# Optimization experiments

Measured on AMD Instinct MI355X. Metric: run time of the kernel, lower is better.

Reference implementation:

```python
import jax, jax.numpy as jnp
import numpy as np

NS, B, T, S, H, V, G = 30, 16, 8, 400, 400, 20000, 3


def setup_inputs() -> dict:
    key = jax.random.key(0)
    ks = jax.random.split(key, 16)
    f = lambda k, shp, s: jax.random.normal(k, shp, jnp.float32) * s
    return dict(
        encoded_hidden=f(ks[0], (B, H), 1.0),
        encoded_outputs=f(ks[1], (B, S, H), 1.0),
        slot_emb=f(ks[2], (NS, H), 0.1),
        emb=f(ks[3], (V, H), 0.1),
        W_ih=f(ks[4], (3 * H, H), 0.05),
        W_hh=f(ks[5], (3 * H, H), 0.05),
        b_ih=jnp.zeros((3 * H,), jnp.float32),
        b_hh=jnp.zeros((3 * H,), jnp.float32),
        W_ratio_w=f(ks[6], (1, 3 * H), 0.05),
        W_ratio_b=jnp.zeros((1,), jnp.float32),
        W_gate_w=f(ks[7], (G, H), 0.05),
        W_gate_b=jnp.zeros((G,), jnp.float32),
        story=jax.random.randint(ks[8], (B, S), 0, V),
        target=jax.random.randint(ks[9], (B, NS, T), 0, V),
        encoded_lens=jax.random.randint(ks[10], (B,), S // 2, S + 1).astype(jnp.int32),
    )


def reference(encoded_hidden, encoded_outputs, slot_emb, emb, W_ih, W_hh, b_ih, b_hh,
              W_ratio_w, W_ratio_b, W_gate_w, W_gate_b, story, target, encoded_lens):
    ns, h = slot_emb.shape
    b, s, _ = encoded_outputs.shape
    t = target.shape[2]
    v = emb.shape[0]
    bs = ns * b  # fused slot*batch decode rows (parallel_decode)

    enc_out = jnp.tile(encoded_outputs, (ns, 1, 1))            # [bs,S,H]
    story_r = jnp.tile(story, (ns, 1))                          # [bs,S]
    lens_r = jnp.tile(encoded_lens, (ns,))                      # [bs]
    mask = jnp.arange(s)[None, :] < lens_r[:, None]             # [bs,S]
    h0 = jnp.tile(encoded_hidden, (ns, 1))                      # [bs,H]
    x0 = jnp.broadcast_to(slot_emb[:, None, :], (ns, b, h)).reshape(bs, h)
    # teacher-forcing inputs, slot-major flatten like target[:, :, wi].T.flatten()
    tf_in = emb[jnp.transpose(target, (2, 1, 0)).reshape(t, bs)]  # [T,bs,H]
    row = jnp.arange(bs)[:, None]
    neg_inf = jnp.float32(-jnp.inf)

    def gru_cell(x, hid):
        gi = x @ W_ih.T + b_ih
        gh = hid @ W_hh.T + b_hh
        ir, iz, inn = jnp.split(gi, 3, axis=-1)
        hr, hz, hn = jnp.split(gh, 3, axis=-1)
        r = jax.nn.sigmoid(ir + hr)
        z = jax.nn.sigmoid(iz + hz)
        n = jnp.tanh(inn + r * hn)
        return (1.0 - z) * n + z * hid

    def step(carry, x_next):
        hid, x = carry
        h_new = gru_cell(x, hid)                                # dec_state == hidden for 1-step GRU
        scores = jnp.einsum('bh,bsh->bs', h_new, enc_out)
        scores = jnp.where(mask, scores, neg_inf)
        prob = jax.nn.softmax(scores, axis=1)
        context = jnp.einsum('bs,bsh->bh', prob, enc_out)
        p_vocab = jax.nn.softmax(h_new @ emb.T, axis=1)         # [bs,V]
        p_gen_vec = jnp.concatenate([h_new, context, x], axis=-1)
        switch = jax.nn.sigmoid(p_gen_vec @ W_ratio_w.T + W_ratio_b)  # [bs,1]
        p_ctx = jnp.zeros((bs, v), p_vocab.dtype).at[row, story_r].add(prob)
        final = (1.0 - switch) * p_ctx + switch * p_vocab
        gate = context @ W_gate_w.T + W_gate_b
        return (h_new, x_next), (final, gate)

    _, (finals, gates) = jax.lax.scan(step, (h0, x0), tf_in)
    all_point = finals.reshape(t, ns, b, v).transpose(1, 2, 0, 3)  # [NS,B,T,V]
    all_gate = gates[0].reshape(ns, b, -1)                          # gates from wi==0
    return all_point, all_gate
```

## Files before the change

kernel.cpp:

```cpp
#include <hip/hip_runtime.h>
#include <hip/hip_bf16.h>

#define NSLOT 30
#define BB    16
#define TT    8
#define SS    400
#define HH    400
#define KP    416
#define NKK   13
#define VV    20000
#define GG    3
#define BSR   480
#define NBN   157
#define NCT   1256
#define FRAG_STRIDE 512

typedef unsigned short u16;
typedef __attribute__((ext_vector_type(8))) short bf16x8;
typedef __attribute__((ext_vector_type(4))) float f32x4;

__device__ __forceinline__ short f2bfs(float f){
  __hip_bfloat16 h = __float2bfloat16(f);
  union { __hip_bfloat16 b; short u; } v; v.b = h; return v.u;
}
__device__ __forceinline__ unsigned int pack2(float lo, float hi){
  return (unsigned int)(u16)f2bfs(lo) | ((unsigned int)(u16)f2bfs(hi) << 16);
}
__device__ __forceinline__ float bfu(u16 u){
  union { unsigned int i; float f; } v; v.i = ((unsigned int)u) << 16; return v.f;
}
__device__ __forceinline__ float sigm(float x){ return 1.f / (1.f + __expf(-x)); }
__device__ __forceinline__ float tanh_fast(float x){
  float e = __expf(2.f * x);
  return 1.f - 2.f / (e + 1.f);
}
__device__ __forceinline__ float wred_max(float v){
  #pragma unroll
  for (int off = 32; off; off >>= 1) v = fmaxf(v, __shfl_xor(v, off, 64));
  return v;
}
__device__ __forceinline__ float wred_sum(float v){
  #pragma unroll
  for (int off = 32; off; off >>= 1) v += __shfl_xor(v, off, 64);
  return v;
}

__global__ __launch_bounds__(256) void k_init(const float* __restrict__ eh,
                                              const float* __restrict__ semb,
                                              float* __restrict__ h_ws,
                                              float* __restrict__ x_ws)
{
  int idx = blockIdx.x * 256 + threadIdx.x;
  if (idx >= BSR * HH) return;
  int r = idx / HH, k = idx - r * HH;
  int batch = r % BB, slot = r / BB;
  h_ws[idx] = eh[batch * HH + k];
  x_ws[idx] = semb[slot * HH + k];
}

__global__ __launch_bounds__(256) void k_cast_emb(const float* __restrict__ emb,
                                                  short* __restrict__ ebf)
{
  const int nunit = NCT * NKK * 64;
  for (int u = blockIdx.x * 256 + threadIdx.x; u < nunit; u += gridDim.x * 256){
    int lane = u & 63;
    int kt = u >> 6;
    int ctile = kt / NKK, kk = kt - ctile * NKK;
    int lg = lane >> 4, cl = lane & 15;
    int c = ctile * 16 + cl;
    int k = kk * 32 + lg * 8;
    bf16x8 o;
    if (c < VV && k < HH){
      const float* src = emb + (size_t)c * HH + k;
      #pragma unroll
      for (int j = 0; j < 8; ++j) o[j] = f2bfs(src[j]);
    } else {
      #pragma unroll
      for (int j = 0; j < 8; ++j) o[j] = 0;
    }
    *reinterpret_cast<bf16x8*>(ebf + (size_t)u * 8) = o;
  }
}

__device__ __forceinline__ void gemm_acc(const float* __restrict__ A,
                                         const float* __restrict__ W,
                                         int N, int v0, int row0, int t,
                                         float acc[4][4])
{
  __shared__ float Af[64][36];
  __shared__ float Bf[64][132];
  const int cidx = t & 31, ridx = t >> 5;
  const int c0 = cidx * 4, r0 = ridx * 4;

  for (int kc = 0; kc < HH; kc += 64){
    const int Kc = (HH - kc >= 64) ? 64 : (HH - kc);
    const int sh = (Kc == 64) ? 4 : 2;
    {
      const int nunit = 32 << sh;
      for (int u = t; u < nunit; u += 256){
        int r = u >> sh;
        int k = (u & ((1 << sh) - 1)) << 2;
        float4 a4 = *reinterpret_cast<const float4*>(A + (size_t)(row0 + r) * HH + kc + k);
        Af[k][r] = a4.x; Af[k+1][r] = a4.y; Af[k+2][r] = a4.z; Af[k+3][r] = a4.w;
      }
    }
    {
      const int nunit = 128 << sh;
      for (int u = t; u < nunit; u += 256){
        int c = u >> sh;
        int k = (u & ((1 << sh) - 1)) << 2;
        float f0 = 0.f, f1 = 0.f, f2 = 0.f, f3 = 0.f;
        int col = v0 + c;
        if (col < N){
          float4 e = *reinterpret_cast<const float4*>(W + (size_t)col * HH + kc + k);
          f0 = e.x; f1 = e.y; f2 = e.z; f3 = e.w;
        }
        Bf[k][c] = f0; Bf[k+1][c] = f1; Bf[k+2][c] = f2; Bf[k+3][c] = f3;
      }
    }
    __syncthreads();
    #pragma unroll 8
    for (int k = 0; k < Kc; ++k){
      float4 a = *reinterpret_cast<const float4*>(&Af[k][r0]);
      float4 b = *reinterpret_cast<const float4*>(&Bf[k][c0]);
      acc[0][0] += a.x*b.x; acc[0][1] += a.x*b.y; acc[0][2] += a.x*b.z; acc[0][3] += a.x*b.w;
      acc[1][0] += a.y*b.x; acc[1][1] += a.y*b.y; acc[1][2] += a.y*b.z; acc[1][3] += a.y*b.w;
      acc[2][0] += a.z*b.x; acc[2][1] += a.z*b.y; acc[2][2] += a.z*b.z; acc[2][3] += a.z*b.w;
      acc[3][0] += a.w*b.x; acc[3][1] += a.w*b.y; acc[3][2] += a.w*b.z; acc[3][3] += a.w*b.w;
    }
    __syncthreads();
  }
}

__global__ __launch_bounds__(256) void k_gemm2(const float* __restrict__ x,
                                               const float* __restrict__ h,
                                               const float* __restrict__ Wih,
                                               const float* __restrict__ Whh,
                                               float* __restrict__ gi,
                                               float* __restrict__ gh, int nb1)
{
  const float* A; const float* W; float* C;
  int bx = blockIdx.x;
  if (bx < nb1){ A = x; W = Wih; C = gi; }
  else         { A = h; W = Whh; C = gh; bx -= nb1; }
  const int N = 3 * HH, v0 = bx * 128, row0 = blockIdx.y * 32, t = threadIdx.x;
  float acc[4][4] = {{0.f}};
  gemm_acc(A, W, N, v0, row0, t, acc);
  const int c0 = (t & 31) * 4, r0 = (t >> 5) * 4;
  #pragma unroll
  for (int i = 0; i < 4; ++i){
    int rr = row0 + r0 + i;
    #pragma unroll
    for (int j = 0; j < 4; ++j){
      int col = v0 + c0 + j;
      if (col < N) C[(size_t)rr * N + col] = acc[i][j];
    }
  }
}

__global__ __launch_bounds__(256) void k_logits_mfma(
    const short* __restrict__ hbf, const short* __restrict__ ebf,
    float* __restrict__ out, float* __restrict__ pmax_ws,
    float* __restrict__ psum_ws, int wi)
{
  const int t = threadIdx.x;
  const int lane = t & 63, wid = t >> 6;
  const int wr = wid >> 1, wc = wid & 1;
  const int l15 = lane & 15, lg = lane >> 4;
  const int bM = blockIdx.x, bN = blockIdx.y;

  const short* ap[4];
  const short* bp[4];
  #pragma unroll
  for (int m = 0; m < 4; ++m){
    int rtile = bM * 8 + wr * 4 + m;
    ap[m] = hbf + (size_t)min(rtile, BSR / 16 - 1) * (NKK * FRAG_STRIDE) + lane * 8;
  }
  #pragma unroll
  for (int n = 0; n < 4; ++n){
    int ctile = bN * 8 + wc * 4 + n;
    bp[n] = ebf + (size_t)ctile * (NKK * FRAG_STRIDE) + lane * 8;
  }

  f32x4 acc[4][4];
  #pragma unroll
  for (int m = 0; m < 4; ++m)
    #pragma unroll
    for (int n = 0; n < 4; ++n)
      acc[m][n] = (f32x4){0.f, 0.f, 0.f, 0.f};

  #pragma unroll
  for (int kk = 0; kk < NKK; ++kk){
    const int ko = kk * FRAG_STRIDE;
    bf16x8 a[4];
    #pragma unroll
    for (int m = 0; m < 4; ++m)
      a[m] = *reinterpret_cast<const bf16x8*>(ap[m] + ko);
    #pragma unroll
    for (int n = 0; n < 4; ++n){
      bf16x8 b = *reinterpret_cast<const bf16x8*>(bp[n] + ko);
      #pragma unroll
      for (int m = 0; m < 4; ++m)
        acc[m][n] = __builtin_amdgcn_mfma_f32_16x16x32_bf16(a[m], b, acc[m][n], 0, 0, 0);
    }
  }

  #pragma unroll
  for (int m = 0; m < 4; ++m){
    #pragma unroll
    for (int q = 0; q < 4; ++q){
      int row = bM * 128 + wr * 64 + m * 16 + lg * 4 + q;
      u16* lrow16 = reinterpret_cast<u16*>(out + ((size_t)row * TT + wi) * VV);
      #pragma unroll
      for (int n = 0; n < 4; ++n){
        float v = acc[m][n][q];
        float vp = __shfl_xor(v, 1, 64);
        int col = bN * 128 + wc * 64 + n * 16 + l15;
        if (((l15 & 1) == 0) && row < BSR && col < VV)
          *reinterpret_cast<unsigned int*>(lrow16 + col) = pack2(v, vp);
      }
    }
    f32x4 rmax, rsum;
    #pragma unroll
    for (int q = 0; q < 4; ++q){
      float mx = -3.0e38f;
      #pragma unroll
      for (int n = 0; n < 4; ++n){
        int col = bN * 128 + wc * 64 + n * 16 + l15;
        float v = (col < VV) ? acc[m][n][q] : -3.0e38f;
        mx = fmaxf(mx, v);
      }
      #pragma unroll
      for (int off = 1; off < 16; off <<= 1) mx = fmaxf(mx, __shfl_xor(mx, off, 64));
      float sm = 0.f;
      #pragma unroll
      for (int n = 0; n < 4; ++n){
        int col = bN * 128 + wc * 64 + n * 16 + l15;
        if (col < VV) sm += __expf(acc[m][n][q] - mx);
      }
      #pragma unroll
      for (int off = 1; off < 16; off <<= 1) sm += __shfl_xor(sm, off, 64);
      rmax[q] = mx; rsum[q] = sm;
    }
    if (l15 == 0){
      #pragma unroll
      for (int q = 0; q < 4; ++q){
        int row = bM * 128 + wr * 64 + m * 16 + lg * 4 + q;
        if (row < BSR){
          size_t pidx = ((size_t)row * NBN + bN) * 2 + wc;
          pmax_ws[pidx] = rmax[q];
          psum_ws[pidx] = rsum[q];
        }
      }
    }
  }
}

__global__ __launch_bounds__(256) void k_att(
    const float* __restrict__ enc, const float* __restrict__ emb,
    const float* __restrict__ b_ih, const float* __restrict__ b_hh,
    const float* __restrict__ Wr_w, const float* __restrict__ Wr_b,
    const float* __restrict__ Wg_w, const float* __restrict__ Wg_b,
    const int* __restrict__ target, const int* __restrict__ lens,
    const float* __restrict__ gi_ws, const float* __restrict__ gh_ws,
    float* __restrict__ h_ws, float* __restrict__ x_ws,
    short* __restrict__ h_bf,
    float* __restrict__ prob_ws, float* __restrict__ sw_ws,
    float* __restrict__ d_out, int wi)
{
  __shared__ float hn_s[HH];
  __shared__ float sc_s[SS];
  __shared__ float ctx_s[HH];
  __shared__ float red[4];
  __shared__ float redg[GG][4];

  const int t = threadIdx.x;
  const int rg = blockIdx.x;
  const int batch = rg % BB, slot = rg / BB;
  const int len = lens[batch];

  const float* gir = gi_ws + (size_t)rg * (3 * HH);
  const float* ghr = gh_ws + (size_t)rg * (3 * HH);
  for (int k = t; k < HH; k += 256){
    float irv = gir[k]          + b_ih[k];
    float izv = gir[HH + k]     + b_ih[HH + k];
    float inv = gir[2 * HH + k] + b_ih[2 * HH + k];
    float hrv = ghr[k]          + b_hh[k];
    float hzv = ghr[HH + k]     + b_hh[HH + k];
    float hnv = ghr[2 * HH + k] + b_hh[2 * HH + k];
    float rr = sigm(irv + hrv);
    float zz = sigm(izv + hzv);
    float nn = tanh_fast(inv + rr * hnv);
    float hold = h_ws[(size_t)rg * HH + k];
    float hnew = (1.f - zz) * nn + zz * hold;
    hn_s[k] = hnew;
    h_ws[(size_t)rg * HH + k] = hnew;
  }
  __syncthreads();

  if (t < KP / 8){
    const int kk = t >> 2, lg = t & 3;
    const int rtile = rg >> 4, rl = rg & 15;
    bf16x8 o;
    #pragma unroll
    for (int j = 0; j < 8; ++j){
      int k = t * 8 + j;
      o[j] = (k < HH) ? f2bfs(hn_s[k]) : (short)0;
    }
    *reinterpret_cast<bf16x8*>(
        h_bf + ((size_t)rtile * NKK + kk) * FRAG_STRIDE + (lg * 16 + rl) * 8) = o;
  }

  const float* encb = enc + (size_t)batch * SS * HH;
  float lmax = -3.0e38f;
  for (int s = t; s < SS; s += 256){
    if (s < len){
      const float4* er4 = reinterpret_cast<const float4*>(encb + (size_t)s * HH);
      float dot = 0.f;
      for (int k4 = 0; k4 < HH / 4; ++k4){
        float4 e = er4[k4];
        float4 hv = *reinterpret_cast<const float4*>(&hn_s[k4 * 4]);
        dot += e.x*hv.x + e.y*hv.y + e.z*hv.z + e.w*hv.w;
      }
      sc_s[s] = dot;
      lmax = fmaxf(lmax, dot);
    }
  }
  lmax = wred_max(lmax);
  if ((t & 63) == 0) red[t >> 6] = lmax;
  __syncthreads();
  lmax = fmaxf(fmaxf(red[0], red[1]), fmaxf(red[2], red[3]));
  float lsum = 0.f;
  for (int s = t; s < SS; s += 256){
    float e = (s < len) ? __expf(sc_s[s] - lmax) : 0.f;
    sc_s[s] = e;
    lsum += e;
  }
  lsum = wred_sum(lsum);
  __syncthreads();
  if ((t & 63) == 0) red[t >> 6] = lsum;
  __syncthreads();
  lsum = red[0] + red[1] + red[2] + red[3];
  float invl = 1.f / lsum;
  for (int s = t; s < SS; s += 256){
    float p = sc_s[s] * invl;
    sc_s[s] = p;
    prob_ws[(size_t)rg * SS + s] = p;
  }
  __syncthreads();

  for (int k = t; k < HH; k += 256){
    float c = 0.f;
    for (int s = 0; s < len; ++s)
      c += sc_s[s] * encb[(size_t)s * HH + k];
    ctx_s[k] = c;
  }
  __syncthreads();

  float sa = 0.f;
  for (int k = t; k < HH; k += 256){
    sa += Wr_w[k]          * hn_s[k]
        + Wr_w[HH + k]     * ctx_s[k]
        + Wr_w[2 * HH + k] * x_ws[(size_t)rg * HH + k];
  }
  sa = wred_sum(sa);
  if ((t & 63) == 0) red[t >> 6] = sa;
  __syncthreads();
  sa = red[0] + red[1] + red[2] + red[3];
  if (t == 0) sw_ws[rg] = sigm(sa + Wr_b[0]);

  if (wi == 0){
    float ga[GG] = {0.f, 0.f, 0.f};
    for (int k = t; k < HH; k += 256){
      float cv = ctx_s[k];
      ga[0] += Wg_w[k] * cv;
      ga[1] += Wg_w[HH + k] * cv;
      ga[2] += Wg_w[2 * HH + k] * cv;
    }
    #pragma unroll
    for (int g = 0; g < GG; ++g){
      ga[g] = wred_sum(ga[g]);
      if ((t & 63) == 0) redg[g][t >> 6] = ga[g];
    }
    __syncthreads();
    if (t < GG)
      d_out[(size_t)NSLOT * BB * TT * VV + (size_t)rg * GG + t] =
          redg[t][0] + redg[t][1] + redg[t][2] + redg[t][3] + Wg_b[t];
  }

  const int tgt = target[batch * (NSLOT * TT) + slot * TT + wi];
  const float* embrow = emb + (size_t)tgt * HH;
  for (int k = t; k < HH; k += 256)
    x_ws[(size_t)rg * HH + k] = embrow[k];
}

__global__ __launch_bounds__(256) void k_finalize(
    float* __restrict__ logits_out, const float* __restrict__ prob_ws,
    const float* __restrict__ pmax_ws, const float* __restrict__ psum_ws,
    const float* __restrict__ sw_ws, const int* __restrict__ story,
    const int* __restrict__ lens, int wi)
{
  __shared__ float pctx[VV];
  __shared__ u16 rowbuf[VV];
  __shared__ float red[4];
  const int t = threadIdx.x;
  const int r = blockIdx.x;
  const int batch = r % BB;
  for (int v = t; v < VV; v += 256) pctx[v] = 0.f;
  __syncthreads();
  const int len = lens[batch];
  for (int s = t; s < SS; s += 256){
    if (s < len)
      atomicAdd(&pctx[story[batch * SS + s]], prob_ws[(size_t)r * SS + s]);
  }

  float* lrow = logits_out + ((size_t)r * TT + wi) * VV;
  const uint4* l16 = reinterpret_cast<const uint4*>(lrow);
  for (int i = t; i < VV / 8; i += 256)
    reinterpret_cast<uint4*>(rowbuf)[i] = l16[i];

  const float* pm = pmax_ws + (size_t)r * (NBN * 2);
  const float* ps = psum_ws + (size_t)r * (NBN * 2);
  float m = -3.0e38f;
  for (int i = t; i < NBN * 2; i += 256) m = fmaxf(m, pm[i]);
  m = wred_max(m);
  if ((t & 63) == 0) red[t >> 6] = m;
  __syncthreads();
  m = fmaxf(fmaxf(red[0], red[1]), fmaxf(red[2], red[3]));
  float lsum = 0.f;
  for (int i = t; i < NBN * 2; i += 256) lsum += ps[i] * __expf(pm[i] - m);
  lsum = wred_sum(lsum);
  __syncthreads();
  if ((t & 63) == 0) red[t >> 6] = lsum;
  __syncthreads();
  lsum = red[0] + red[1] + red[2] + red[3];

  const float sw = sw_ws[r];
  const float invl = sw / lsum;
  const float osw = 1.f - sw;
  float4* o4 = reinterpret_cast<float4*>(lrow);
  for (int i = t; i < VV / 4; i += 256){
    ushort4 s4 = reinterpret_cast<const ushort4*>(rowbuf)[i];
    int v = i * 4;
    float4 o;
    o.x = __expf(bfu(s4.x) - m) * invl + osw * pctx[v + 0];
    o.y = __expf(bfu(s4.y) - m) * invl + osw * pctx[v + 1];
    o.z = __expf(bfu(s4.z) - m) * invl + osw * pctx[v + 2];
    o.w = __expf(bfu(s4.w) - m) * invl + osw * pctx[v + 3];
    o4[i] = o;
  }
}

extern "C" void kernel_launch(void* const* d_in, const int* in_sizes, int n_in,
                              void* d_out, int out_size, void* d_ws, size_t ws_size,
                              hipStream_t stream)
{
  (void)in_sizes; (void)n_in; (void)out_size; (void)ws_size;
  const float* eh    = (const float*)d_in[0];
  const float* enc   = (const float*)d_in[1];
  const float* semb  = (const float*)d_in[2];
  const float* emb   = (const float*)d_in[3];
  const float* W_ih  = (const float*)d_in[4];
  const float* W_hh  = (const float*)d_in[5];
  const float* b_ih  = (const float*)d_in[6];
  const float* b_hh  = (const float*)d_in[7];
  const float* Wr_w  = (const float*)d_in[8];
  const float* Wr_b  = (const float*)d_in[9];
  const float* Wg_w  = (const float*)d_in[10];
  const float* Wg_b  = (const float*)d_in[11];
  const int* story = (const int*)d_in[12];
  const int* tgt   = (const int*)d_in[13];
  const int* lens  = (const int*)d_in[14];
  float* out = (float*)d_out;

  float* ws      = (float*)d_ws;
  float* h_ws    = ws;
  float* x_ws    = ws + 192000;
  float* prob_ws = ws + 384000;
  float* sw_ws   = ws + 576000;
  float* gi_ws   = ws + 576512;
  float* gh_ws   = ws + 1152512;
  float* pmax_ws = ws + 1728512;
  float* psum_ws = ws + 1879552;
  short* h_bf    = (short*)(ws + 2030592);
  short* emb_bf  = (short*)(ws + 2130432);

  k_cast_emb<<<2048, 256, 0, stream>>>(emb, emb_bf);
  k_init<<<750, 256, 0, stream>>>(eh, semb, h_ws, x_ws);
  for (int wi = 0; wi < TT; ++wi){
    dim3 gg(20, 15);
    k_gemm2<<<gg, 256, 0, stream>>>(x_ws, h_ws, W_ih, W_hh, gi_ws, gh_ws, 10);
    k_att<<<BSR, 256, 0, stream>>>(enc, emb, b_ih, b_hh, Wr_w, Wr_b, Wg_w, Wg_b,
                                   tgt, lens, gi_ws, gh_ws, h_ws, x_ws, h_bf,
                                   prob_ws, sw_ws, out, wi);
    dim3 gl(4, NBN);
    k_logits_mfma<<<gl, 256, 0, stream>>>(h_bf, emb_bf, out, pmax_ws, psum_ws, wi);
    k_finalize<<<BSR, 256, 0, stream>>>(out, prob_ws, pmax_ws, psum_ws,
                                        sw_ws, story, lens, wi);
  }
}
```

Measured before the change: 1.144 ms.

## Move GRU gate GEMMs to bf16x3 split-precision MFMA with pre-cast fragments

Replaces the fp32 LDS-tiled SIMT GEMM for the GRU input and hidden projections with an MFMA kernel. Operands are split into bf16 hi and lo parts and multiplied with three MFMAs to keep close to fp32 accuracy. Weights are pre-cast once into fragment layout, and the attention kernel now writes h and x fragments directly for the next step. The context reduction loop is also unrolled by four with separate accumulators, which shortens dependency chains. The cost is extra cast kernels, more workspace, and three times the MFMA work.

```diff
diff --git a/kernel.cpp b/kernel.cpp
--- a/kernel.cpp
+++ b/kernel.cpp
@@ -13,6 +13,9 @@
 #define BSR   480
 #define NBN   157
 #define NCT   1256
+#define NG2   1200
+#define NCT2  75
+#define NRT   30
 #define FRAG_STRIDE 512
 
 typedef unsigned short u16;
@@ -56,6 +59,66 @@
   int batch = r % BB, slot = r / BB;
   h_ws[idx] = eh[batch * HH + k];
   x_ws[idx] = semb[slot * HH + k];
+}
+
+__global__ __launch_bounds__(256) void k_split_xh(
+    const float* __restrict__ h_ws, const float* __restrict__ x_ws,
+    short* __restrict__ h_hi, short* __restrict__ h_lo,
+    short* __restrict__ x_hi, short* __restrict__ x_lo)
+{
+  const int NU = NRT * NKK * 64;
+  for (int u = blockIdx.x * 256 + threadIdx.x; u < 2 * NU; u += gridDim.x * 256){
+    int uu = u; int sel = 0;
+    if (uu >= NU){ uu -= NU; sel = 1; }
+    const float* S = sel ? x_ws : h_ws;
+    short* ph = sel ? x_hi : h_hi;
+    short* pl = sel ? x_lo : h_lo;
+    int lane = uu & 63, kt = uu >> 6;
+    int rtile = kt / NKK, kk = kt - rtile * NKK;
+    int lg = lane >> 4, rl = lane & 15;
+    int r = rtile * 16 + rl, k = kk * 32 + lg * 8;
+    bf16x8 oh, ol;
+    #pragma unroll
+    for (int j = 0; j < 8; ++j){
+      if (k + j < HH){
+        float v = S[(size_t)r * HH + k + j];
+        short hb = f2bfs(v);
+        oh[j] = hb; ol[j] = f2bfs(v - bfu((u16)hb));
+      } else { oh[j] = 0; ol[j] = 0; }
+    }
+    *reinterpret_cast<bf16x8*>(ph + (size_t)uu * 8) = oh;
+    *reinterpret_cast<bf16x8*>(pl + (size_t)uu * 8) = ol;
+  }
+}
+
+__global__ __launch_bounds__(256) void k_cast_W(
+    const float* __restrict__ Wih, const float* __restrict__ Whh,
+    short* __restrict__ Wih_hi, short* __restrict__ Wih_lo,
+    short* __restrict__ Whh_hi, short* __restrict__ Whh_lo)
+{
+  const int NU = NCT2 * NKK * 64;
+  for (int u = blockIdx.x * 256 + threadIdx.x; u < 2 * NU; u += gridDim.x * 256){
+    int uu = u; int sel = 0;
+    if (uu >= NU){ uu -= NU; sel = 1; }
+    const float* W = sel ? Whh : Wih;
+    short* ph = sel ? Whh_hi : Wih_hi;
+    short* pl = sel ? Whh_lo : Wih_lo;
+    int lane = uu & 63, kt = uu >> 6;
+    int ctile = kt / NKK, kk = kt - ctile * NKK;
+    int lg = lane >> 4, cl = lane & 15;
+    int c = ctile * 16 + cl, k = kk * 32 + lg * 8;
+    bf16x8 oh, ol;
+    #pragma unroll
+    for (int j = 0; j < 8; ++j){
+      if (k + j < HH){
+        float v = W[(size_t)c * HH + k + j];
+        short hb = f2bfs(v);
+        oh[j] = hb; ol[j] = f2bfs(v - bfu((u16)hb));
+      } else { oh[j] = 0; ol[j] = 0; }
+    }
+    *reinterpret_cast<bf16x8*>(ph + (size_t)uu * 8) = oh;
+    *reinterpret_cast<bf16x8*>(pl + (size_t)uu * 8) = ol;
+  }
 }
 
 __global__ __launch_bounds__(256) void k_cast_emb(const float* __restrict__ emb,
@@ -82,78 +145,80 @@
   }
 }
 
-__device__ __forceinline__ void gemm_acc(const float* __restrict__ A,
-                                         const float* __restrict__ W,
-                                         int N, int v0, int row0, int t,
-                                         float acc[4][4])
-{
-  __shared__ float Af[64][36];
-  __shared__ float Bf[64][132];
-  const int cidx = t & 31, ridx = t >> 5;
-  const int c0 = cidx * 4, r0 = ridx * 4;
-
-  for (int kc = 0; kc < HH; kc += 64){
-    const int Kc = (HH - kc >= 64) ? 64 : (HH - kc);
-    const int sh = (Kc == 64) ? 4 : 2;
-    {
-      const int nunit = 32 << sh;
-      for (int u = t; u < nunit; u += 256){
-        int r = u >> sh;
-        int k = (u & ((1 << sh) - 1)) << 2;
-        float4 a4 = *reinterpret_cast<const float4*>(A + (size_t)(row0 + r) * HH + kc + k);
-        Af[k][r] = a4.x; Af[k+1][r] = a4.y; Af[k+2][r] = a4.z; Af[k+3][r] = a4.w;
+__global__ __launch_bounds__(256) void k_gemm2_mfma(
+    const short* __restrict__ x_hi, const short* __restrict__ x_lo,
+    const short* __restrict__ h_hi, const short* __restrict__ h_lo,
+    const short* __restrict__ Wih_hi, const short* __restrict__ Wih_lo,
+    const short* __restrict__ Whh_hi, const short* __restrict__ Whh_lo,
+    float* __restrict__ gi, float* __restrict__ gh)
+{
+  const int t = threadIdx.x;
+  const int lane = t & 63, wid = t >> 6;
+  const int wr = wid >> 1, wc = wid & 1;
+  const int l15 = lane & 15, lg = lane >> 4;
+  const int bM = blockIdx.x, bN = blockIdx.y, z = blockIdx.z;
+
+  const short* A_hi = z ? h_hi : x_hi;
+  const short* A_lo = z ? h_lo : x_lo;
+  const short* B_hi = z ? Whh_hi : Wih_hi;
+  const short* B_lo = z ? Whh_lo : Wih_lo;
+  float* C = z ? gh : gi;
+
+  const short *ah[4], *al[4], *bh[4], *bl[4];
+  #pragma unroll
+  for (int m = 0; m < 4; ++m){
+    int rtile = min(bM * 8 + wr * 4 + m, NRT - 1);
+    size_t off = (size_t)rtile * (NKK * FRAG_STRIDE) + lane * 8;
+    ah[m] = A_hi + off; al[m] = A_lo + off;
+  }
+  #pragma unroll
+  for (int n = 0; n < 4; ++n){
+    int ctile = min(bN * 8 + wc * 4 + n, NCT2 - 1);
+    size_t off = (size_t)ctile * (NKK * FRAG_STRIDE) + lane * 8;
+    bh[n] = B_hi + off; bl[n] = B_lo + off;
+  }
+
+  f32x4 acc[4][4];
+  #pragma unroll
+  for (int m = 0; m < 4; ++m)
+    #pragma unroll
+    for (int n = 0; n < 4; ++n)
+      acc[m][n] = (f32x4){0.f, 0.f, 0.f, 0.f};
+
+  #pragma unroll
+  for (int kk = 0; kk < NKK; ++kk){
+    const int ko = kk * FRAG_STRIDE;
+    bf16x8 ah_r[4], al_r[4];
+    #pragma unroll
+    for (int m = 0; m < 4; ++m){
+      ah_r[m] = *reinterpret_cast<const bf16x8*>(ah[m] + ko);
+      al_r[m] = *reinterpret_cast<const bf16x8*>(al[m] + ko);
+    }
+    #pragma unroll
+    for (int n = 0; n < 4; ++n){
+      bf16x8 bhv = *reinterpret_cast<const bf16x8*>(bh[n] + ko);
+      bf16x8 blv = *reinterpret_cast<const bf16x8*>(bl[n] + ko);
+      #pragma unroll
+      for (int m = 0; m < 4; ++m){
+        acc[m][n] = __builtin_amdgcn_mfma_f32_16x16x32_bf16(ah_r[m], bhv, acc[m][n], 0, 0, 0);
+        acc[m][n] = __builtin_amdgcn_mfma_f32_16x16x32_bf16(ah_r[m], blv, acc[m][n], 0, 0, 0);
+        acc[m][n] = __builtin_amdgcn_mfma_f32_16x16x32_bf16(al_r[m], bhv, acc[m][n], 0, 0, 0);
       }
     }
-    {
-      const int nunit = 128 << sh;
-      for (int u = t; u < nunit; u += 256){
-        int c = u >> sh;
-        int k = (u & ((1 << sh) - 1)) << 2;
-        float f0 = 0.f, f1 = 0.f, f2 = 0.f, f3 = 0.f;
-        int col = v0 + c;
-        if (col < N){
-          float4 e = *reinterpret_cast<const float4*>(W + (size_t)col * HH + kc + k);
-          f0 = e.x; f1 = e.y; f2 = e.z; f3 = e.w;
+  }
+
+  #pragma unroll
+  for (int m = 0; m < 4; ++m){
+    #pragma unroll
+    for (int q = 0; q < 4; ++q){
+      int row = bM * 128 + wr * 64 + m * 16 + lg * 4 + q;
+      if (row < BSR){
+        #pragma unroll
+        for (int n = 0; n < 4; ++n){
+          int col = bN * 128 + wc * 64 + n * 16 + l15;
+          if (col < NG2) C[(size_t)row * NG2 + col] = acc[m][n][q];
         }
-        Bf[k][c] = f0; Bf[k+1][c] = f1; Bf[k+2][c] = f2; Bf[k+3][c] = f3;
       }
-    }
-    __syncthreads();
-    #pragma unroll 8
-    for (int k = 0; k < Kc; ++k){
-      float4 a = *reinterpret_cast<const float4*>(&Af[k][r0]);
-      float4 b = *reinterpret_cast<const float4*>(&Bf[k][c0]);
-      acc[0][0] += a.x*b.x; acc[0][1] += a.x*b.y; acc[0][2] += a.x*b.z; acc[0][3] += a.x*b.w;
-      acc[1][0] += a.y*b.x; acc[1][1] += a.y*b.y; acc[1][2] += a.y*b.z; acc[1][3] += a.y*b.w;
-      acc[2][0] += a.z*b.x; acc[2][1] += a.z*b.y; acc[2][2] += a.z*b.z; acc[2][3] += a.z*b.w;
-      acc[3][0] += a.w*b.x; acc[3][1] += a.w*b.y; acc[3][2] += a.w*b.z; acc[3][3] += a.w*b.w;
-    }
-    __syncthreads();
-  }
-}
-
-__global__ __launch_bounds__(256) void k_gemm2(const float* __restrict__ x,
-                                               const float* __restrict__ h,
-                                               const float* __restrict__ Wih,
-                                               const float* __restrict__ Whh,
-                                               float* __restrict__ gi,
-                                               float* __restrict__ gh, int nb1)
-{
-  const float* A; const float* W; float* C;
-  int bx = blockIdx.x;
-  if (bx < nb1){ A = x; W = Wih; C = gi; }
-  else         { A = h; W = Whh; C = gh; bx -= nb1; }
-  const int N = 3 * HH, v0 = bx * 128, row0 = blockIdx.y * 32, t = threadIdx.x;
-  float acc[4][4] = {{0.f}};
-  gemm_acc(A, W, N, v0, row0, t, acc);
-  const int c0 = (t & 31) * 4, r0 = (t >> 5) * 4;
-  #pragma unroll
-  for (int i = 0; i < 4; ++i){
-    int rr = row0 + r0 + i;
-    #pragma unroll
-    for (int j = 0; j < 4; ++j){
-      int col = v0 + c0 + j;
-      if (col < N) C[(size_t)rr * N + col] = acc[i][j];
     }
   }
 }
@@ -174,7 +239,7 @@
   #pragma unroll
   for (int m = 0; m < 4; ++m){
     int rtile = bM * 8 + wr * 4 + m;
-    ap[m] = hbf + (size_t)min(rtile, BSR / 16 - 1) * (NKK * FRAG_STRIDE) + lane * 8;
+    ap[m] = hbf + (size_t)min(rtile, NRT - 1) * (NKK * FRAG_STRIDE) + lane * 8;
   }
   #pragma unroll
   for (int n = 0; n < 4; ++n){
@@ -264,7 +329,8 @@
     const int* __restrict__ target, const int* __restrict__ lens,
     const float* __restrict__ gi_ws, const float* __restrict__ gh_ws,
     float* __restrict__ h_ws, float* __restrict__ x_ws,
-    short* __restrict__ h_bf,
+    short* __restrict__ h_hi, short* __restrict__ h_lo,
+    short* __restrict__ x_hi, short* __restrict__ x_lo,
     float* __restrict__ prob_ws, float* __restrict__ sw_ws,
     float* __restrict__ d_out, int wi)
 {
@@ -278,9 +344,10 @@
   const int rg = blockIdx.x;
   const int batch = rg % BB, slot = rg / BB;
   const int len = lens[batch];
-
-  const float* gir = gi_ws + (size_t)rg * (3 * HH);
-  const float* ghr = gh_ws + (size_t)rg * (3 * HH);
+  const int rtile = rg >> 4, rl = rg & 15;
+
+  const float* gir = gi_ws + (size_t)rg * NG2;
+  const float* ghr = gh_ws + (size_t)rg * NG2;
   for (int k = t; k < HH; k += 256){
     float irv = gir[k]          + b_ih[k];
     float izv = gir[HH + k]     + b_ih[HH + k];
@@ -300,15 +367,19 @@
 
   if (t < KP / 8){
     const int kk = t >> 2, lg = t & 3;
-    const int rtile = rg >> 4, rl = rg & 15;
-    bf16x8 o;
+    bf16x8 oh, ol;
     #pragma unroll
     for (int j = 0; j < 8; ++j){
       int k = t * 8 + j;
-      o[j] = (k < HH) ? f2bfs(hn_s[k]) : (short)0;
-    }
-    *reinterpret_cast<bf16x8*>(
-        h_bf + ((size_t)rtile * NKK + kk) * FRAG_STRIDE + (lg * 16 + rl) * 8) = o;
+      if (k < HH){
+        float v = hn_s[k];
+        short hb = f2bfs(v);
+        oh[j] = hb; ol[j] = f2bfs(v - bfu((u16)hb));
+      } else { oh[j] = 0; ol[j] = 0; }
+    }
+    size_t off = ((size_t)rtile * NKK + kk) * FRAG_STRIDE + (lg * 16 + rl) * 8;
+    *reinterpret_cast<bf16x8*>(h_hi + off) = oh;
+    *reinterpret_cast<bf16x8*>(h_lo + off) = ol;
   }
 
   const float* encb = enc + (size_t)batch * SS * HH;
@@ -350,10 +421,17 @@
   __syncthreads();
 
   for (int k = t; k < HH; k += 256){
-    float c = 0.f;
-    for (int s = 0; s < len; ++s)
-      c += sc_s[s] * encb[(size_t)s * HH + k];
-    ctx_s[k] = c;
+    float c0 = 0.f, c1 = 0.f, c2 = 0.f, c3 = 0.f;
+    const float* ek = encb + k;
+    int s = 0;
+    for (; s + 3 < len; s += 4){
+      c0 += sc_s[s]     * ek[(size_t)s * HH];
+      c1 += sc_s[s + 1] * ek[(size_t)(s + 1) * HH];
+      c2 += sc_s[s + 2] * ek[(size_t)(s + 2) * HH];
+      c3 += sc_s[s + 3] * ek[(size_t)(s + 3) * HH];
+    }
+    for (; s < len; ++s) c0 += sc_s[s] * ek[(size_t)s * HH];
+    ctx_s[k] = (c0 + c1) + (c2 + c3);
   }
   __syncthreads();
 
@@ -392,6 +470,22 @@
   const float* embrow = emb + (size_t)tgt * HH;
   for (int k = t; k < HH; k += 256)
     x_ws[(size_t)rg * HH + k] = embrow[k];
+  if (t < KP / 8){
+    const int kk = t >> 2, lg = t & 3;
+    bf16x8 oh, ol;
+    #pragma unroll
+    for (int j = 0; j < 8; ++j){
+      int k = t * 8 + j;
+      if (k < HH){
+        float v = embrow[k];
+        short hb = f2bfs(v);
+        oh[j] = hb; ol[j] = f2bfs(v - bfu((u16)hb));
+      } else { oh[j] = 0; ol[j] = 0; }
+    }
+    size_t off = ((size_t)rtile * NKK + kk) * FRAG_STRIDE + (lg * 16 + rl) * 8;
+    *reinterpret_cast<bf16x8*>(x_hi + off) = oh;
+    *reinterpret_cast<bf16x8*>(x_lo + off) = ol;
+  }
 }
 
 __global__ __launch_bounds__(256) void k_finalize(
@@ -482,19 +576,31 @@
   float* gh_ws   = ws + 1152512;
   float* pmax_ws = ws + 1728512;
   float* psum_ws = ws + 1879552;
-  short* h_bf    = (short*)(ws + 2030592);
+  short* h_hi    = (short*)(ws + 2030592);
   short* emb_bf  = (short*)(ws + 2130432);
+  short* Wih_hi  = (short*)(ws + 6310400);
+  short* Wih_lo  = (short*)(ws + 6560000);
+  short* Whh_hi  = (short*)(ws + 6809600);
+  short* Whh_lo  = (short*)(ws + 7059200);
+  short* x_hi    = (short*)(ws + 7308800);
+  short* x_lo    = (short*)(ws + 7408640);
+  short* h_lo    = (short*)(ws + 7508480);
 
   k_cast_emb<<<2048, 256, 0, stream>>>(emb, emb_bf);
+  k_cast_W<<<512, 256, 0, stream>>>(W_ih, W_hh, Wih_hi, Wih_lo, Whh_hi, Whh_lo);
   k_init<<<750, 256, 0, stream>>>(eh, semb, h_ws, x_ws);
+  k_split_xh<<<195, 256, 0, stream>>>(h_ws, x_ws, h_hi, h_lo, x_hi, x_lo);
   for (int wi = 0; wi < TT; ++wi){
-    dim3 gg(20, 15);
-    k_gemm2<<<gg, 256, 0, stream>>>(x_ws, h_ws, W_ih, W_hh, gi_ws, gh_ws, 10);
+    dim3 gg(4, 10, 2);
+    k_gemm2_mfma<<<gg, 256, 0, stream>>>(x_hi, x_lo, h_hi, h_lo,
+                                         Wih_hi, Wih_lo, Whh_hi, Whh_lo,
+                                         gi_ws, gh_ws);
     k_att<<<BSR, 256, 0, stream>>>(enc, emb, b_ih, b_hh, Wr_w, Wr_b, Wg_w, Wg_b,
-                                   tgt, lens, gi_ws, gh_ws, h_ws, x_ws, h_bf,
+                                   tgt, lens, gi_ws, gh_ws, h_ws, x_ws,
+                                   h_hi, h_lo, x_hi, x_lo,
                                    prob_ws, sw_ws, out, wi);
     dim3 gl(4, NBN);
-    k_logits_mfma<<<gl, 256, 0, stream>>>(h_bf, emb_bf, out, pmax_ws, psum_ws, wi);
+    k_logits_mfma<<<gl, 256, 0, stream>>>(h_hi, emb_bf, out, pmax_ws, psum_ws, wi);
     k_finalize<<<BSR, 256, 0, stream>>>(out, prob_ws, pmax_ws, psum_ws,
                                         sw_ws, story, lens, wi);
   }
```

After: 1.017 ms. 1.12x faster.
